# Performance work log

Measured on AMD Instinct MI355X. Metric: run time of the kernel, lower is better.

The kernel has to match this reference:

```python
import jax, jax.numpy as jnp
import numpy as np

H = 2048      # hidden_size
E = 16        # num_experts
I = 512       # moe_intermediate_size
IS = 2048     # shared_expert_intermediate_size
TOP_K = 2
B, S = 1, 2048


def setup_inputs() -> dict:
    key = jax.random.key(0)
    ks = jax.random.split(key, 9)
    std = 0.02
    return {
        "hidden_states": jax.random.normal(ks[0], (B, S, H), dtype=jnp.float32),
        "gate_w": jax.random.normal(ks[1], (E, H), dtype=jnp.float32) * std,
        "w1": jax.random.normal(ks[2], (E, I, H), dtype=jnp.float32) * std,  # gate_proj per expert
        "w2": jax.random.normal(ks[3], (E, H, I), dtype=jnp.float32) * std,  # down_proj per expert
        "w3": jax.random.normal(ks[4], (E, I, H), dtype=jnp.float32) * std,  # up_proj per expert
        "ws_gate": jax.random.normal(ks[5], (IS, H), dtype=jnp.float32) * std,  # shared gate_proj
        "ws_up": jax.random.normal(ks[6], (IS, H), dtype=jnp.float32) * std,    # shared up_proj
        "ws_down": jax.random.normal(ks[7], (H, IS), dtype=jnp.float32) * std,  # shared down_proj
        "shared_gate_w": jax.random.normal(ks[8], (1, H), dtype=jnp.float32) * std,
    }


def reference(hidden_states, gate_w, w1, w2, w3, ws_gate, ws_up, ws_down, shared_gate_w):
    b, s, h = hidden_states.shape
    x = hidden_states.reshape(-1, h)                     # [T, H]
    T = x.shape[0]

    # Router: softmax in fp32, top-k, renormalize (norm_topk_prob=True)
    router_logits = x @ gate_w.T                         # [T, E]
    routing = jax.nn.softmax(router_logits.astype(jnp.float32), axis=-1)
    topw, sel = jax.lax.top_k(routing, TOP_K)            # [T, K]
    topw = topw / jnp.sum(topw, axis=-1, keepdims=True)
    topw = topw.astype(x.dtype)

    # Scatter top-k weights into dense [T, E] combine matrix (torch_moe semantics)
    combine = jnp.zeros((T, E), dtype=x.dtype).at[jnp.arange(T)[:, None], sel].set(topw)

    # Expert SwiGLU MLPs evaluated densely, masked/weighted by combine
    hmid = jax.nn.silu(jnp.einsum('th,eih->tei', x, w1)) * jnp.einsum('th,eih->tei', x, w3)  # [T,E,I]
    hmid = hmid * combine[:, :, None]
    moe_out = jnp.einsum('tei,ehi->th', hmid, w2)        # [T, H]

    # Shared expert with sigmoid gate
    shared = (jax.nn.silu(x @ ws_gate.T) * (x @ ws_up.T)) @ ws_down.T  # [T, H]
    shared = jax.nn.sigmoid(x @ shared_gate_w.T) * shared

    return (moe_out + shared).reshape(b, s, h)
```

## Files before the change

### kernel.cpp

```cpp
#include <hip/hip_runtime.h>
#include <hip/hip_bf16.h>
#include <cmath>

#define HDIM 2048
#define NEXP 16
#define IDIM 512
#define ISDIM 2048
#define NTOK 2048
#define MAXTILES 80
#define ROWSCAP (MAXTILES * 64)

#define GU_NBLK_EXP (MAXTILES * 4)
#define GU_NBLK_SH ((NTOK / 64) * (ISDIM / 128))
#define DN_NBLK_EXP (MAXTILES * 8)
#define DN_NBLK_SH ((NTOK / 64) * (HDIM / 256))

typedef short bf16x8 __attribute__((ext_vector_type(8)));
typedef float f32x4 __attribute__((ext_vector_type(4)));
typedef unsigned short us;
typedef __attribute__((address_space(1))) const unsigned int* as1p;
typedef __attribute__((address_space(3))) unsigned int* as3p;

__device__ __forceinline__ us f2bf(float f) {
  unsigned int u = __builtin_bit_cast(unsigned int, f);
  u += 0x7FFFu + ((u >> 16) & 1u);
  return (us)(u >> 16);
}

__device__ __forceinline__ void glds16(const void* g, void* l) {
  __builtin_amdgcn_global_load_lds((as1p)(unsigned long long)g,
                                   (as3p)(unsigned int)(unsigned long long)l, 16, 0, 0);
}

struct SrcPtrs { const float* p[6]; };
__global__ __launch_bounds__(256) void k_convert(SrcPtrs s, us* __restrict__ dst) {
  int b = blockIdx.x;
  const float* sp;
  long long rel;
  size_t doff;
  if (b < 8192)       { sp = s.p[0]; rel = b;         doff = 0; }
  else if (b < 16384) { sp = s.p[1]; rel = b - 8192;  doff = 16777216; }
  else if (b < 24576) { sp = s.p[2]; rel = b - 16384; doff = 33554432; }
  else if (b < 26624) { sp = s.p[3]; rel = b - 24576; doff = 50331648; }
  else if (b < 28672) { sp = s.p[4]; rel = b - 26624; doff = 54525952; }
  else                { sp = s.p[5]; rel = b - 28672; doff = 58720256; }
  size_t i8 = (size_t)rel * 2048 + threadIdx.x * 8;
  float4 a = ((const float4*)sp)[i8 >> 2];
  float4 c = ((const float4*)sp)[(i8 >> 2) + 1];
  bf16x8 v = {(short)f2bf(a.x), (short)f2bf(a.y), (short)f2bf(a.z), (short)f2bf(a.w),
              (short)f2bf(c.x), (short)f2bf(c.y), (short)f2bf(c.z), (short)f2bf(c.w)};
  *(bf16x8*)(dst + doff + i8) = v;
}

__global__ __launch_bounds__(256) void k_router(const float* __restrict__ x,
                                                const float* __restrict__ gate_w,
                                                const float* __restrict__ sgw,
                                                us* __restrict__ xb,
                                                int* __restrict__ sel,
                                                float* __restrict__ wnorm,
                                                float* __restrict__ sig,
                                                int* __restrict__ counts) {
  __shared__ float lg[4][17];
  int tid = threadIdx.x, wid = tid >> 6, lane = tid & 63;
  int t = blockIdx.x * 4 + wid;
  const float4* xrow = reinterpret_cast<const float4*>(x + (size_t)t * HDIM);
  float4 xv[8];
#pragma unroll
  for (int s = 0; s < 8; s++) xv[s] = xrow[s * 64 + lane];
  ushort4* xbrow = reinterpret_cast<ushort4*>(xb + (size_t)t * HDIM);
#pragma unroll
  for (int s = 0; s < 8; s++) {
    ushort4 o;
    o.x = f2bf(xv[s].x); o.y = f2bf(xv[s].y); o.z = f2bf(xv[s].z); o.w = f2bf(xv[s].w);
    xbrow[s * 64 + lane] = o;
  }
#pragma unroll 1
  for (int e = 0; e < 17; e++) {
    const float4* gr =
        reinterpret_cast<const float4*>(e < 16 ? gate_w + (size_t)e * HDIM : sgw);
    float acc = 0.f;
#pragma unroll
    for (int s = 0; s < 8; s++) {
      float4 g = gr[s * 64 + lane];
      acc += xv[s].x * g.x + xv[s].y * g.y + xv[s].z * g.z + xv[s].w * g.w;
    }
#pragma unroll
    for (int off = 32; off; off >>= 1) acc += __shfl_xor(acc, off, 64);
    if (lane == 0) lg[wid][e] = acc;
  }
  if (lane == 0) {
    float* L = lg[wid];
    int i1 = 0; float v1 = L[0];
    for (int i = 1; i < NEXP; i++) if (L[i] > v1) { v1 = L[i]; i1 = i; }
    int i2 = (i1 == 0) ? 1 : 0; float v2 = L[i2];
    for (int i = 0; i < NEXP; i++)
      if (i != i1 && i != i2 && L[i] > v2) { v2 = L[i]; i2 = i; }
    float wa = 1.f / (1.f + expf(v2 - v1));
    sel[2 * t] = i1; sel[2 * t + 1] = i2;
    wnorm[2 * t] = wa; wnorm[2 * t + 1] = 1.f - wa;
    sig[t] = 1.f / (1.f + expf(-L[16]));
    atomicAdd(&counts[i1], 1);
    atomicAdd(&counts[i2], 1);
  }
}

__global__ __launch_bounds__(256) void k_scan_scatter(const int* __restrict__ counts,
                                                      const int* __restrict__ sel,
                                                      const float* __restrict__ wnorm,
                                                      int* __restrict__ tile_expert,
                                                      int* __restrict__ row_token,
                                                      int* __restrict__ rowk,
                                                      float* __restrict__ rw) {
  __shared__ int offs_s[NEXP];
  __shared__ int fill_s[NEXP];
  int tid = threadIdx.x;
  for (int r = tid; r < ROWSCAP; r += 256) row_token[r] = -1;
  if (tid < NEXP) fill_s[tid] = 0;
  if (tid == 0) {
    int acc = 0;
    for (int e = 0; e < NEXP; e++) {
      offs_s[e] = acc;
      int nt = (counts[e] + 63) >> 6;
      for (int i = 0; i < nt; i++) tile_expert[(acc >> 6) + i] = e;
      acc += nt << 6;
    }
    for (int m = acc >> 6; m < MAXTILES; m++) tile_expert[m] = -1;
  }
  __syncthreads();
  for (int t = tid; t < NTOK; t += 256) {
    for (int k = 0; k < 2; k++) {
      int e = sel[2 * t + k];
      int pos = atomicAdd(&fill_s[e], 1);
      int row = offs_s[e] + pos;
      row_token[row] = t;
      rowk[row] = k;
      rw[row] = wnorm[2 * t + k];
    }
  }
}

__global__ __launch_bounds__(256) void k_gu(
    const us* __restrict__ xb, const us* __restrict__ wb1, const us* __restrict__ wb3,
    const us* __restrict__ wsgb, const us* __restrict__ wsub,
    const int* __restrict__ tile_expert, const int* __restrict__ row_token,
    us* __restrict__ hmid, us* __restrict__ hs) {
  __shared__ us As[64 * 64];
  __shared__ us Bg[128 * 64];
  __shared__ us Bu[128 * 64];
  int bid = blockIdx.x, tid = threadIdx.x;
  int w = tid >> 6, lane = tid & 63;
  int lr = lane >> 3, lc = lane & 7;
  int arow0 = w * 16 + lr, arow1 = arow0 + 8;
  const us *bG, *bU;
  us* outp;
  int mt, n0, ostride, tok0, tok1;
  if (bid < GU_NBLK_EXP) {
    mt = bid >> 2; int nt = bid & 3;
    int e = tile_expert[mt];
    if (e < 0) return;
    int a = row_token[mt * 64 + arow0];
    int b = row_token[mt * 64 + arow1];
    tok0 = a < 0 ? 0 : a;
    tok1 = b < 0 ? 0 : b;
    bG = wb1 + ((size_t)e * IDIM + nt * 128) * HDIM;
    bU = wb3 + ((size_t)e * IDIM + nt * 128) * HDIM;
    outp = hmid; ostride = IDIM; n0 = nt * 128;
  } else {
    int sb = bid - GU_NBLK_EXP;
    mt = sb >> 4; int nt = sb & 15;
    tok0 = mt * 64 + arow0;
    tok1 = mt * 64 + arow1;
    bG = wsgb + (size_t)(nt * 128) * HDIM;
    bU = wsub + (size_t)(nt * 128) * HDIM;
    outp = hs; ostride = ISDIM; n0 = nt * 128;
  }
  int quad = lane >> 4, l16 = lane & 15, sw = l16 & 7;
  int swz = (lc ^ lr) * 8;
  const us* aSrc0 = xb + (size_t)tok0 * HDIM + swz;
  const us* aSrc1 = xb + (size_t)tok1 * HDIM + swz;
  size_t bLaneOff = (size_t)lr * HDIM + swz;
  f32x4 accG[4][2] = {};
  f32x4 accU[4][2] = {};
  for (int k0 = 0; k0 < HDIM; k0 += 64) {
    glds16(aSrc0 + k0, As + (size_t)(w * 2) * 512);
    glds16(aSrc1 + k0, As + (size_t)(w * 2 + 1) * 512);
#pragma unroll
    for (int ii = 0; ii < 8; ii++) {
      int i = w * 8 + ii;
      int g = i & 15;
      if (i < 16)
        glds16(bG + (size_t)g * 8 * HDIM + bLaneOff + k0, Bg + (size_t)g * 512);
      else
        glds16(bU + (size_t)g * 8 * HDIM + bLaneOff + k0, Bu + (size_t)g * 512);
    }
    __syncthreads();
#pragma unroll
    for (int ks = 0; ks < 2; ks++) {
      int cb = (ks * 4 + quad) ^ sw;
      bf16x8 af[4], bg[2], bu[2];
#pragma unroll
      for (int ms = 0; ms < 4; ms++)
        af[ms] = *(const bf16x8*)&As[((ms * 16 + l16) * 8 + cb) * 8];
#pragma unroll
      for (int ns = 0; ns < 2; ns++) {
        int n = w * 32 + ns * 16 + l16;
        bg[ns] = *(const bf16x8*)&Bg[(n * 8 + cb) * 8];
        bu[ns] = *(const bf16x8*)&Bu[(n * 8 + cb) * 8];
      }
#pragma unroll
      for (int ms = 0; ms < 4; ms++)
#pragma unroll
        for (int ns = 0; ns < 2; ns++) {
          accG[ms][ns] = __builtin_amdgcn_mfma_f32_16x16x32_bf16(af[ms], bg[ns], accG[ms][ns], 0, 0, 0);
          accU[ms][ns] = __builtin_amdgcn_mfma_f32_16x16x32_bf16(af[ms], bu[ns], accU[ms][ns], 0, 0, 0);
        }
    }
    __syncthreads();
  }
#pragma unroll
  for (int ms = 0; ms < 4; ms++)
#pragma unroll
    for (int ns = 0; ns < 2; ns++)
#pragma unroll
      for (int r = 0; r < 4; r++) {
        float g = accG[ms][ns][r], u = accU[ms][ns][r];
        float hv = (g / (1.f + __expf(-g))) * u;
        int row = mt * 64 + ms * 16 + quad * 4 + r;
        int col = n0 + w * 32 + ns * 16 + l16;
        outp[(size_t)row * ostride + col] = f2bf(hv);
      }
}

__global__ __launch_bounds__(256) void k_down(
    const us* __restrict__ hmid, const us* __restrict__ hs,
    const us* __restrict__ wb2, const us* __restrict__ wsdb,
    const int* __restrict__ tile_expert, const int* __restrict__ row_token,
    const int* __restrict__ rowk, const float* __restrict__ rw,
    const float* __restrict__ sig, us* __restrict__ slab) {
  __shared__ us As[64 * 64];
  __shared__ us Bs[256 * 64];
  __shared__ long long idx_s[64];
  __shared__ float wgt_s[64];
  int bid = blockIdx.x, tid = threadIdx.x;
  int w = tid >> 6, lane = tid & 63;
  const us *aBase, *bBase;
  int K, mt, n0;
  if (bid < DN_NBLK_EXP) {
    mt = bid >> 3; int nt = bid & 7;
    int e = tile_expert[mt];
    if (e < 0) return;
    aBase = hmid + (size_t)mt * 64 * IDIM; K = IDIM;
    bBase = wb2 + ((size_t)e * HDIM + nt * 256) * IDIM;
    n0 = nt * 256;
    if (tid < 64) {
      int tk = row_token[mt * 64 + tid];
      if (tk < 0) { idx_s[tid] = -1; wgt_s[tid] = 0.f; }
      else {
        idx_s[tid] = ((long long)rowk[mt * 64 + tid] * NTOK + tk) * HDIM;
        wgt_s[tid] = rw[mt * 64 + tid];
      }
    }
  } else {
    int sb = bid - DN_NBLK_EXP;
    mt = sb >> 3; int nt = sb & 7;
    aBase = hs + (size_t)mt * 64 * ISDIM; K = ISDIM;
    bBase = wsdb + (size_t)(nt * 256) * ISDIM;
    n0 = nt * 256;
    if (tid < 64) {
      int t = mt * 64 + tid;
      idx_s[tid] = (2LL * NTOK + t) * (long long)HDIM;
      wgt_s[tid] = sig[t];
    }
  }
  int quad = lane >> 4, l16 = lane & 15, sw = l16 & 7;
  int lr = lane >> 3, lc = lane & 7;
  int swz = (lc ^ lr) * 8;
  const us* aSrc0 = aBase + (size_t)(w * 16 + lr) * K + swz;
  const us* aSrc1 = aBase + (size_t)(w * 16 + 8 + lr) * K + swz;
  size_t bLaneOff = (size_t)lr * K + swz;
  f32x4 acc[4][4] = {};
  for (int k0 = 0; k0 < K; k0 += 64) {
    glds16(aSrc0 + k0, As + (size_t)(w * 2) * 512);
    glds16(aSrc1 + k0, As + (size_t)(w * 2 + 1) * 512);
#pragma unroll
    for (int ii = 0; ii < 8; ii++) {
      int g = w * 8 + ii;
      glds16(bBase + (size_t)g * 8 * K + bLaneOff + k0, Bs + (size_t)g * 512);
    }
    __syncthreads();
#pragma unroll
    for (int ks = 0; ks < 2; ks++) {
      int cb = (ks * 4 + quad) ^ sw;
      bf16x8 af[4], bf[4];
#pragma unroll
      for (int ms = 0; ms < 4; ms++)
        af[ms] = *(const bf16x8*)&As[((ms * 16 + l16) * 8 + cb) * 8];
#pragma unroll
      for (int ns = 0; ns < 4; ns++) {
        int n = w * 64 + ns * 16 + l16;
        bf[ns] = *(const bf16x8*)&Bs[(n * 8 + cb) * 8];
      }
#pragma unroll
      for (int ms = 0; ms < 4; ms++)
#pragma unroll
        for (int ns = 0; ns < 4; ns++)
          acc[ms][ns] = __builtin_amdgcn_mfma_f32_16x16x32_bf16(af[ms], bf[ns], acc[ms][ns], 0, 0, 0);
    }
    __syncthreads();
  }
#pragma unroll
  for (int ms = 0; ms < 4; ms++)
#pragma unroll
    for (int r = 0; r < 4; r++) {
      int rr = ms * 16 + quad * 4 + r;
      long long ix = idx_s[rr];
      if (ix >= 0) {
        float wgt = wgt_s[rr];
        us* orow = slab + ix + n0 + w * 64;
#pragma unroll
        for (int ns = 0; ns < 4; ns++)
          orow[ns * 16 + l16] = f2bf(wgt * acc[ms][ns][r]);
      }
    }
}

__global__ __launch_bounds__(256) void k_combine(const us* __restrict__ slab,
                                                 float* __restrict__ out) {
  size_t i = ((size_t)blockIdx.x * 256 + threadIdx.x) * 8;
  bf16x8 a = *(const bf16x8*)(slab + i);
  bf16x8 b = *(const bf16x8*)(slab + (size_t)NTOK * HDIM + i);
  bf16x8 c = *(const bf16x8*)(slab + 2 * (size_t)NTOK * HDIM + i);
  float4 o[2];
#pragma unroll
  for (int j = 0; j < 8; j++) {
    float fa = __builtin_bit_cast(float, (unsigned)((unsigned)(us)a[j] << 16));
    float fb = __builtin_bit_cast(float, (unsigned)((unsigned)(us)b[j] << 16));
    float fc = __builtin_bit_cast(float, (unsigned)((unsigned)(us)c[j] << 16));
    ((float*)o)[j] = fa + fb + fc;
  }
  *(float4*)(out + i) = o[0];
  *(float4*)(out + i + 4) = o[1];
}

extern "C" void kernel_launch(void* const* d_in, const int* in_sizes, int n_in,
                              void* d_out, int out_size, void* d_ws, size_t ws_size,
                              hipStream_t stream) {
  const float* x = (const float*)d_in[0];
  const float* gate_w = (const float*)d_in[1];
  const float* w1 = (const float*)d_in[2];
  const float* w2 = (const float*)d_in[3];
  const float* w3 = (const float*)d_in[4];
  const float* wsg = (const float*)d_in[5];
  const float* wsu = (const float*)d_in[6];
  const float* wsd = (const float*)d_in[7];
  const float* sgw = (const float*)d_in[8];
  float* out = (float*)d_out;

  us* xb = (us*)d_ws;
  us* hs = xb + (size_t)NTOK * HDIM;
  us* hmid = hs + (size_t)NTOK * ISDIM;
  us* wb1 = hmid + (size_t)ROWSCAP * IDIM;
  us* wb3 = wb1 + (size_t)16777216;
  us* wb2 = wb3 + (size_t)16777216;
  us* wsgb = wb2 + (size_t)16777216;
  us* wsub = wsgb + (size_t)4194304;
  us* wsdb = wsub + (size_t)4194304;
  us* slab = wsdb + (size_t)4194304;
  float* rw = (float*)(slab + (size_t)3 * 4194304);
  float* wnorm = rw + ROWSCAP;
  float* sig = wnorm + 2 * NTOK;
  int* sel = (int*)(sig + NTOK);
  int* row_token = sel + 2 * NTOK;
  int* rowk = row_token + ROWSCAP;
  int* counts = rowk + ROWSCAP;
  int* tile_expert = counts + NEXP;

  SrcPtrs sp;
  sp.p[0] = w1; sp.p[1] = w3; sp.p[2] = w2;
  sp.p[3] = wsg; sp.p[4] = wsu; sp.p[5] = wsd;

  hipMemsetAsync(counts, 0, NEXP * sizeof(int), stream);
  k_convert<<<dim3(30720), dim3(256), 0, stream>>>(sp, wb1);
  k_router<<<dim3(NTOK / 4), dim3(256), 0, stream>>>(x, gate_w, sgw, xb, sel, wnorm,
                                                     sig, counts);
  k_scan_scatter<<<dim3(1), dim3(256), 0, stream>>>(counts, sel, wnorm, tile_expert,
                                                    row_token, rowk, rw);
  k_gu<<<dim3(GU_NBLK_EXP + GU_NBLK_SH), dim3(256), 0, stream>>>(
      xb, wb1, wb3, wsgb, wsub, tile_expert, row_token, hmid, hs);
  k_down<<<dim3(DN_NBLK_EXP + DN_NBLK_SH), dim3(256), 0, stream>>>(
      hmid, hs, wb2, wsdb, tile_expert, row_token, rowk, rw, sig, slab);
  k_combine<<<dim3(NTOK * HDIM / 2048), dim3(256), 0, stream>>>(slab, out);
}
```

Baseline: 512.9 us.

## Fuse fp32-to-bf16 weight conversion into GEMM staging with 128-row tiles

```diff
diff --git a/kernel.cpp b/kernel.cpp
--- a/kernel.cpp
+++ b/kernel.cpp
@@ -7,13 +7,13 @@
 #define IDIM 512
 #define ISDIM 2048
 #define NTOK 2048
-#define MAXTILES 80
-#define ROWSCAP (MAXTILES * 64)
-
-#define GU_NBLK_EXP (MAXTILES * 4)
-#define GU_NBLK_SH ((NTOK / 64) * (ISDIM / 128))
-#define DN_NBLK_EXP (MAXTILES * 8)
-#define DN_NBLK_SH ((NTOK / 64) * (HDIM / 256))
+#define MAXT 48
+#define ROWSCAP (MAXT * 128)
+
+#define GU_EXP (MAXT * 4)
+#define GU_SH ((NTOK / 128) * (ISDIM / 128))
+#define DN_SH ((NTOK / 128) * (HDIM / 256))
+#define DN_EXP (MAXT * 8)
 
 typedef short bf16x8 __attribute__((ext_vector_type(8)));
 typedef float f32x4 __attribute__((ext_vector_type(4)));
@@ -26,30 +26,33 @@
   u += 0x7FFFu + ((u >> 16) & 1u);
   return (us)(u >> 16);
 }
+__device__ __forceinline__ float bf2f(us v) {
+  return __builtin_bit_cast(float, (unsigned)v << 16);
+}
 
 __device__ __forceinline__ void glds16(const void* g, void* l) {
   __builtin_amdgcn_global_load_lds((as1p)(unsigned long long)g,
                                    (as3p)(unsigned int)(unsigned long long)l, 16, 0, 0);
 }
 
-struct SrcPtrs { const float* p[6]; };
-__global__ __launch_bounds__(256) void k_convert(SrcPtrs s, us* __restrict__ dst) {
-  int b = blockIdx.x;
-  const float* sp;
-  long long rel;
-  size_t doff;
-  if (b < 8192)       { sp = s.p[0]; rel = b;         doff = 0; }
-  else if (b < 16384) { sp = s.p[1]; rel = b - 8192;  doff = 16777216; }
-  else if (b < 24576) { sp = s.p[2]; rel = b - 16384; doff = 33554432; }
-  else if (b < 26624) { sp = s.p[3]; rel = b - 24576; doff = 50331648; }
-  else if (b < 28672) { sp = s.p[4]; rel = b - 26624; doff = 54525952; }
-  else                { sp = s.p[5]; rel = b - 28672; doff = 58720256; }
-  size_t i8 = (size_t)rel * 2048 + threadIdx.x * 8;
-  float4 a = ((const float4*)sp)[i8 >> 2];
-  float4 c = ((const float4*)sp)[(i8 >> 2) + 1];
-  bf16x8 v = {(short)f2bf(a.x), (short)f2bf(a.y), (short)f2bf(a.z), (short)f2bf(a.w),
-              (short)f2bf(c.x), (short)f2bf(c.y), (short)f2bf(c.z), (short)f2bf(c.w)};
-  *(bf16x8*)(dst + doff + i8) = v;
+__device__ __forceinline__ void stage_cvt(const float* __restrict__ src,
+                                          us* __restrict__ dst) {
+  const float4* p = (const float4*)src;
+  float4 a = p[0], b = p[1];
+  unsigned u0 = __builtin_bit_cast(unsigned, a.x) + 0x8000u;
+  unsigned u1 = __builtin_bit_cast(unsigned, a.y) + 0x8000u;
+  unsigned u2 = __builtin_bit_cast(unsigned, a.z) + 0x8000u;
+  unsigned u3 = __builtin_bit_cast(unsigned, a.w) + 0x8000u;
+  unsigned u4 = __builtin_bit_cast(unsigned, b.x) + 0x8000u;
+  unsigned u5 = __builtin_bit_cast(unsigned, b.y) + 0x8000u;
+  unsigned u6 = __builtin_bit_cast(unsigned, b.z) + 0x8000u;
+  unsigned u7 = __builtin_bit_cast(unsigned, b.w) + 0x8000u;
+  int4 v;
+  v.x = __builtin_amdgcn_perm(u1, u0, 0x07060302);
+  v.y = __builtin_amdgcn_perm(u3, u2, 0x07060302);
+  v.z = __builtin_amdgcn_perm(u5, u4, 0x07060302);
+  v.w = __builtin_amdgcn_perm(u7, u6, 0x07060302);
+  *(int4*)dst = v;
 }
 
 __global__ __launch_bounds__(256) void k_router(const float* __restrict__ x,
@@ -120,11 +123,11 @@
     int acc = 0;
     for (int e = 0; e < NEXP; e++) {
       offs_s[e] = acc;
-      int nt = (counts[e] + 63) >> 6;
-      for (int i = 0; i < nt; i++) tile_expert[(acc >> 6) + i] = e;
-      acc += nt << 6;
-    }
-    for (int m = acc >> 6; m < MAXTILES; m++) tile_expert[m] = -1;
+      int nt = (counts[e] + 127) >> 7;
+      for (int i = 0; i < nt; i++) tile_expert[(acc >> 7) + i] = e;
+      acc += nt << 7;
+    }
+    for (int m = acc >> 7; m < MAXT; m++) tile_expert[m] = -1;
   }
   __syncthreads();
   for (int t = tid; t < NTOK; t += 256) {
@@ -139,153 +142,167 @@
   }
 }
 
-__global__ __launch_bounds__(256) void k_gu(
-    const us* __restrict__ xb, const us* __restrict__ wb1, const us* __restrict__ wb3,
-    const us* __restrict__ wsgb, const us* __restrict__ wsub,
-    const int* __restrict__ tile_expert, const int* __restrict__ row_token,
-    us* __restrict__ hmid, us* __restrict__ hs) {
-  __shared__ us As[64 * 64];
-  __shared__ us Bg[128 * 64];
-  __shared__ us Bu[128 * 64];
+__global__ __launch_bounds__(512) void k_gu(
+    const us* __restrict__ xb, const float* __restrict__ w1,
+    const float* __restrict__ w3, const float* __restrict__ wsg,
+    const float* __restrict__ wsu, const int* __restrict__ tile_expert,
+    const int* __restrict__ row_token, us* __restrict__ hmid,
+    us* __restrict__ hs) {
+  __shared__ us As[128 * 64];
+  __shared__ us Bs[2][128 * 64];
+  __shared__ int toks_s[128];
   int bid = blockIdx.x, tid = threadIdx.x;
   int w = tid >> 6, lane = tid & 63;
-  int lr = lane >> 3, lc = lane & 7;
-  int arow0 = w * 16 + lr, arow1 = arow0 + 8;
-  const us *bG, *bU;
+  const float *bG, *bU;
   us* outp;
-  int mt, n0, ostride, tok0, tok1;
-  if (bid < GU_NBLK_EXP) {
+  int mt, n0, ostride;
+  if (bid < GU_EXP) {
     mt = bid >> 2; int nt = bid & 3;
     int e = tile_expert[mt];
     if (e < 0) return;
-    int a = row_token[mt * 64 + arow0];
-    int b = row_token[mt * 64 + arow1];
-    tok0 = a < 0 ? 0 : a;
-    tok1 = b < 0 ? 0 : b;
-    bG = wb1 + ((size_t)e * IDIM + nt * 128) * HDIM;
-    bU = wb3 + ((size_t)e * IDIM + nt * 128) * HDIM;
+    if (tid < 128) {
+      int tk = row_token[mt * 128 + tid];
+      toks_s[tid] = tk < 0 ? 0 : tk;
+    }
+    bG = w1 + ((size_t)e * IDIM + nt * 128) * HDIM;
+    bU = w3 + ((size_t)e * IDIM + nt * 128) * HDIM;
     outp = hmid; ostride = IDIM; n0 = nt * 128;
   } else {
-    int sb = bid - GU_NBLK_EXP;
+    int sb = bid - GU_EXP;
     mt = sb >> 4; int nt = sb & 15;
-    tok0 = mt * 64 + arow0;
-    tok1 = mt * 64 + arow1;
-    bG = wsgb + (size_t)(nt * 128) * HDIM;
-    bU = wsub + (size_t)(nt * 128) * HDIM;
+    if (tid < 128) toks_s[tid] = mt * 128 + tid;
+    bG = wsg + (size_t)(nt * 128) * HDIM;
+    bU = wsu + (size_t)(nt * 128) * HDIM;
     outp = hs; ostride = ISDIM; n0 = nt * 128;
   }
+  __syncthreads();
+  int lr = lane >> 3, lc = lane & 7;
+  int swz = (lc ^ lr) * 8;
+  const us* aSrc0 = xb + (size_t)toks_s[w * 16 + lr] * HDIM + swz;
+  const us* aSrc1 = xb + (size_t)toks_s[w * 16 + 8 + lr] * HDIM + swz;
+  int r0 = tid >> 3, p0 = tid & 7, g0 = p0 ^ (r0 & 7);
+  int r1 = (tid + 512) >> 3, g1 = p0 ^ (r1 & 7);
+  size_t bo0 = (size_t)r0 * HDIM + g0 * 8;
+  size_t bo1 = (size_t)r1 * HDIM + g1 * 8;
+  int mat = w >> 2, sub = w & 3, wm = sub >> 1, wn = sub & 1;
   int quad = lane >> 4, l16 = lane & 15, sw = l16 & 7;
-  int swz = (lc ^ lr) * 8;
-  const us* aSrc0 = xb + (size_t)tok0 * HDIM + swz;
-  const us* aSrc1 = xb + (size_t)tok1 * HDIM + swz;
-  size_t bLaneOff = (size_t)lr * HDIM + swz;
-  f32x4 accG[4][2] = {};
-  f32x4 accU[4][2] = {};
+  f32x4 acc[4][4] = {};
   for (int k0 = 0; k0 < HDIM; k0 += 64) {
-    glds16(aSrc0 + k0, As + (size_t)(w * 2) * 512);
-    glds16(aSrc1 + k0, As + (size_t)(w * 2 + 1) * 512);
-#pragma unroll
-    for (int ii = 0; ii < 8; ii++) {
-      int i = w * 8 + ii;
-      int g = i & 15;
-      if (i < 16)
-        glds16(bG + (size_t)g * 8 * HDIM + bLaneOff + k0, Bg + (size_t)g * 512);
-      else
-        glds16(bU + (size_t)g * 8 * HDIM + bLaneOff + k0, Bu + (size_t)g * 512);
-    }
+    glds16(aSrc0 + k0, As + w * 1024);
+    glds16(aSrc1 + k0, As + w * 1024 + 512);
+    stage_cvt(bG + bo0 + k0, &Bs[0][(r0 * 8 + p0) * 8]);
+    stage_cvt(bG + bo1 + k0, &Bs[0][(r1 * 8 + p0) * 8]);
+    stage_cvt(bU + bo0 + k0, &Bs[1][(r0 * 8 + p0) * 8]);
+    stage_cvt(bU + bo1 + k0, &Bs[1][(r1 * 8 + p0) * 8]);
     __syncthreads();
 #pragma unroll
     for (int ks = 0; ks < 2; ks++) {
       int cb = (ks * 4 + quad) ^ sw;
-      bf16x8 af[4], bg[2], bu[2];
+      bf16x8 af[4], bf[4];
 #pragma unroll
       for (int ms = 0; ms < 4; ms++)
-        af[ms] = *(const bf16x8*)&As[((ms * 16 + l16) * 8 + cb) * 8];
-#pragma unroll
-      for (int ns = 0; ns < 2; ns++) {
-        int n = w * 32 + ns * 16 + l16;
-        bg[ns] = *(const bf16x8*)&Bg[(n * 8 + cb) * 8];
-        bu[ns] = *(const bf16x8*)&Bu[(n * 8 + cb) * 8];
-      }
+        af[ms] = *(const bf16x8*)&As[((wm * 64 + ms * 16 + l16) * 8 + cb) * 8];
+#pragma unroll
+      for (int ns = 0; ns < 4; ns++)
+        bf[ns] = *(const bf16x8*)&Bs[mat][((wn * 64 + ns * 16 + l16) * 8 + cb) * 8];
 #pragma unroll
       for (int ms = 0; ms < 4; ms++)
 #pragma unroll
-        for (int ns = 0; ns < 2; ns++) {
-          accG[ms][ns] = __builtin_amdgcn_mfma_f32_16x16x32_bf16(af[ms], bg[ns], accG[ms][ns], 0, 0, 0);
-          accU[ms][ns] = __builtin_amdgcn_mfma_f32_16x16x32_bf16(af[ms], bu[ns], accU[ms][ns], 0, 0, 0);
+        for (int ns = 0; ns < 4; ns++)
+          acc[ms][ns] = __builtin_amdgcn_mfma_f32_16x16x32_bf16(af[ms], bf[ns], acc[ms][ns], 0, 0, 0);
+    }
+    __syncthreads();
+  }
+  us* ub = (us*)Bs;
+  if (mat == 1) {
+#pragma unroll
+    for (int ms = 0; ms < 4; ms++)
+#pragma unroll
+      for (int ns = 0; ns < 4; ns++)
+#pragma unroll
+        for (int r = 0; r < 4; r++) {
+          int row = wm * 64 + ms * 16 + quad * 4 + r;
+          int col = wn * 64 + ns * 16 + l16;
+          ub[row * 128 + col] = f2bf(acc[ms][ns][r]);
         }
-    }
-    __syncthreads();
-  }
-#pragma unroll
-  for (int ms = 0; ms < 4; ms++)
-#pragma unroll
-    for (int ns = 0; ns < 2; ns++)
-#pragma unroll
-      for (int r = 0; r < 4; r++) {
-        float g = accG[ms][ns][r], u = accU[ms][ns][r];
-        float hv = (g / (1.f + __expf(-g))) * u;
-        int row = mt * 64 + ms * 16 + quad * 4 + r;
-        int col = n0 + w * 32 + ns * 16 + l16;
-        outp[(size_t)row * ostride + col] = f2bf(hv);
-      }
-}
-
-__global__ __launch_bounds__(256) void k_down(
+  }
+  __syncthreads();
+  if (mat == 0) {
+#pragma unroll
+    for (int ms = 0; ms < 4; ms++)
+#pragma unroll
+      for (int ns = 0; ns < 4; ns++)
+#pragma unroll
+        for (int r = 0; r < 4; r++) {
+          int row = wm * 64 + ms * 16 + quad * 4 + r;
+          int col = wn * 64 + ns * 16 + l16;
+          float g = acc[ms][ns][r];
+          float u = bf2f(ub[row * 128 + col]);
+          float hv = (g / (1.f + __expf(-g))) * u;
+          outp[(size_t)(mt * 128 + row) * ostride + n0 + col] = f2bf(hv);
+        }
+  }
+}
+
+__global__ __launch_bounds__(512) void k_down(
     const us* __restrict__ hmid, const us* __restrict__ hs,
-    const us* __restrict__ wb2, const us* __restrict__ wsdb,
+    const float* __restrict__ w2, const float* __restrict__ wsd,
     const int* __restrict__ tile_expert, const int* __restrict__ row_token,
     const int* __restrict__ rowk, const float* __restrict__ rw,
     const float* __restrict__ sig, us* __restrict__ slab) {
-  __shared__ us As[64 * 64];
+  __shared__ us As[128 * 64];
   __shared__ us Bs[256 * 64];
-  __shared__ long long idx_s[64];
-  __shared__ float wgt_s[64];
+  __shared__ int idx_s[128];
+  __shared__ float wgt_s[128];
   int bid = blockIdx.x, tid = threadIdx.x;
   int w = tid >> 6, lane = tid & 63;
-  const us *aBase, *bBase;
+  const us* aBase;
+  const float* bBase;
   int K, mt, n0;
-  if (bid < DN_NBLK_EXP) {
+  if (bid < DN_SH) {
     mt = bid >> 3; int nt = bid & 7;
+    aBase = hs + (size_t)mt * 128 * ISDIM; K = ISDIM;
+    bBase = wsd + (size_t)(nt * 256) * ISDIM;
+    n0 = nt * 256;
+    if (tid < 128) {
+      int t = mt * 128 + tid;
+      idx_s[tid] = 2 * NTOK * HDIM + t * HDIM;
+      wgt_s[tid] = sig[t];
+    }
+  } else {
+    int sb = bid - DN_SH;
+    mt = sb >> 3; int nt = sb & 7;
     int e = tile_expert[mt];
     if (e < 0) return;
-    aBase = hmid + (size_t)mt * 64 * IDIM; K = IDIM;
-    bBase = wb2 + ((size_t)e * HDIM + nt * 256) * IDIM;
+    aBase = hmid + (size_t)mt * 128 * IDIM; K = IDIM;
+    bBase = w2 + ((size_t)e * HDIM + nt * 256) * IDIM;
     n0 = nt * 256;
-    if (tid < 64) {
-      int tk = row_token[mt * 64 + tid];
+    if (tid < 128) {
+      int tk = row_token[mt * 128 + tid];
       if (tk < 0) { idx_s[tid] = -1; wgt_s[tid] = 0.f; }
       else {
-        idx_s[tid] = ((long long)rowk[mt * 64 + tid] * NTOK + tk) * HDIM;
-        wgt_s[tid] = rw[mt * 64 + tid];
+        idx_s[tid] = (rowk[mt * 128 + tid] * NTOK + tk) * HDIM;
+        wgt_s[tid] = rw[mt * 128 + tid];
       }
     }
-  } else {
-    int sb = bid - DN_NBLK_EXP;
-    mt = sb >> 3; int nt = sb & 7;
-    aBase = hs + (size_t)mt * 64 * ISDIM; K = ISDIM;
-    bBase = wsdb + (size_t)(nt * 256) * ISDIM;
-    n0 = nt * 256;
-    if (tid < 64) {
-      int t = mt * 64 + tid;
-      idx_s[tid] = (2LL * NTOK + t) * (long long)HDIM;
-      wgt_s[tid] = sig[t];
-    }
-  }
-  int quad = lane >> 4, l16 = lane & 15, sw = l16 & 7;
+  }
+  __syncthreads();
   int lr = lane >> 3, lc = lane & 7;
   int swz = (lc ^ lr) * 8;
   const us* aSrc0 = aBase + (size_t)(w * 16 + lr) * K + swz;
   const us* aSrc1 = aBase + (size_t)(w * 16 + 8 + lr) * K + swz;
-  size_t bLaneOff = (size_t)lr * K + swz;
+  int r0 = tid >> 3, p0 = tid & 7;
+  int wmn = w >> 2, wn = w & 3;
+  int quad = lane >> 4, l16 = lane & 15, sw = l16 & 7;
   f32x4 acc[4][4] = {};
   for (int k0 = 0; k0 < K; k0 += 64) {
-    glds16(aSrc0 + k0, As + (size_t)(w * 2) * 512);
-    glds16(aSrc1 + k0, As + (size_t)(w * 2 + 1) * 512);
-#pragma unroll
-    for (int ii = 0; ii < 8; ii++) {
-      int g = w * 8 + ii;
-      glds16(bBase + (size_t)g * 8 * K + bLaneOff + k0, Bs + (size_t)g * 512);
+    glds16(aSrc0 + k0, As + w * 1024);
+    glds16(aSrc1 + k0, As + w * 1024 + 512);
+#pragma unroll
+    for (int j = 0; j < 4; j++) {
+      int row = r0 + j * 64;
+      int gc = p0 ^ (row & 7);
+      stage_cvt(bBase + (size_t)row * K + gc * 8 + k0, &Bs[(row * 8 + p0) * 8]);
     }
     __syncthreads();
 #pragma unroll
@@ -294,12 +311,10 @@
       bf16x8 af[4], bf[4];
 #pragma unroll
       for (int ms = 0; ms < 4; ms++)
-        af[ms] = *(const bf16x8*)&As[((ms * 16 + l16) * 8 + cb) * 8];
-#pragma unroll
-      for (int ns = 0; ns < 4; ns++) {
-        int n = w * 64 + ns * 16 + l16;
-        bf[ns] = *(const bf16x8*)&Bs[(n * 8 + cb) * 8];
-      }
+        af[ms] = *(const bf16x8*)&As[((wmn * 64 + ms * 16 + l16) * 8 + cb) * 8];
+#pragma unroll
+      for (int ns = 0; ns < 4; ns++)
+        bf[ns] = *(const bf16x8*)&Bs[((wn * 64 + ns * 16 + l16) * 8 + cb) * 8];
 #pragma unroll
       for (int ms = 0; ms < 4; ms++)
 #pragma unroll
@@ -312,11 +327,11 @@
   for (int ms = 0; ms < 4; ms++)
 #pragma unroll
     for (int r = 0; r < 4; r++) {
-      int rr = ms * 16 + quad * 4 + r;
-      long long ix = idx_s[rr];
+      int rr = wmn * 64 + ms * 16 + quad * 4 + r;
+      int ix = idx_s[rr];
       if (ix >= 0) {
         float wgt = wgt_s[rr];
-        us* orow = slab + ix + n0 + w * 64;
+        us* orow = slab + (size_t)ix + n0 + wn * 64;
 #pragma unroll
         for (int ns = 0; ns < 4; ns++)
           orow[ns * 16 + l16] = f2bf(wgt * acc[ms][ns][r]);
@@ -332,12 +347,8 @@
   bf16x8 c = *(const bf16x8*)(slab + 2 * (size_t)NTOK * HDIM + i);
   float4 o[2];
 #pragma unroll
-  for (int j = 0; j < 8; j++) {
-    float fa = __builtin_bit_cast(float, (unsigned)((unsigned)(us)a[j] << 16));
-    float fb = __builtin_bit_cast(float, (unsigned)((unsigned)(us)b[j] << 16));
-    float fc = __builtin_bit_cast(float, (unsigned)((unsigned)(us)c[j] << 16));
-    ((float*)o)[j] = fa + fb + fc;
-  }
+  for (int j = 0; j < 8; j++)
+    ((float*)o)[j] = bf2f((us)a[j]) + bf2f((us)b[j]) + bf2f((us)c[j]);
   *(float4*)(out + i) = o[0];
   *(float4*)(out + i + 4) = o[1];
 }
@@ -359,14 +370,8 @@
   us* xb = (us*)d_ws;
   us* hs = xb + (size_t)NTOK * HDIM;
   us* hmid = hs + (size_t)NTOK * ISDIM;
-  us* wb1 = hmid + (size_t)ROWSCAP * IDIM;
-  us* wb3 = wb1 + (size_t)16777216;
-  us* wb2 = wb3 + (size_t)16777216;
-  us* wsgb = wb2 + (size_t)16777216;
-  us* wsub = wsgb + (size_t)4194304;
-  us* wsdb = wsub + (size_t)4194304;
-  us* slab = wsdb + (size_t)4194304;
-  float* rw = (float*)(slab + (size_t)3 * 4194304);
+  us* slab = hmid + (size_t)ROWSCAP * IDIM;
+  float* rw = (float*)(slab + (size_t)3 * NTOK * HDIM);
   float* wnorm = rw + ROWSCAP;
   float* sig = wnorm + 2 * NTOK;
   int* sel = (int*)(sig + NTOK);
@@ -375,19 +380,14 @@
   int* counts = rowk + ROWSCAP;
   int* tile_expert = counts + NEXP;
 
-  SrcPtrs sp;
-  sp.p[0] = w1; sp.p[1] = w3; sp.p[2] = w2;
-  sp.p[3] = wsg; sp.p[4] = wsu; sp.p[5] = wsd;
-
   hipMemsetAsync(counts, 0, NEXP * sizeof(int), stream);
-  k_convert<<<dim3(30720), dim3(256), 0, stream>>>(sp, wb1);
   k_router<<<dim3(NTOK / 4), dim3(256), 0, stream>>>(x, gate_w, sgw, xb, sel, wnorm,
                                                      sig, counts);
   k_scan_scatter<<<dim3(1), dim3(256), 0, stream>>>(counts, sel, wnorm, tile_expert,
                                                     row_token, rowk, rw);
-  k_gu<<<dim3(GU_NBLK_EXP + GU_NBLK_SH), dim3(256), 0, stream>>>(
-      xb, wb1, wb3, wsgb, wsub, tile_expert, row_token, hmid, hs);
-  k_down<<<dim3(DN_NBLK_EXP + DN_NBLK_SH), dim3(256), 0, stream>>>(
-      hmid, hs, wb2, wsdb, tile_expert, row_token, rowk, rw, sig, slab);
+  k_gu<<<dim3(GU_EXP + GU_SH), dim3(512), 0, stream>>>(
+      xb, w1, w3, wsg, wsu, tile_expert, row_token, hmid, hs);
+  k_down<<<dim3(DN_SH + DN_EXP), dim3(512), 0, stream>>>(
+      hmid, hs, w2, wsd, tile_expert, row_token, rowk, rw, sig, slab);
   k_combine<<<dim3(NTOK * HDIM / 2048), dim3(256), 0, stream>>>(slab, out);
 }
```

New measurement: 459.9 us. -10.4%, faster.
